# Performance work log

Measured on AMD Instinct MI355X. Metric: run time of the kernel, lower is better.

Reference implementation:

```python
import jax, jax.numpy as jnp
import numpy as np

DT = 1.0
BETA_E = float(np.exp(-DT / 20.0))
BETA_I = float(np.exp(-DT / 10.0))
ALPHA_E = float(np.exp(-DT / 5.0))
ALPHA_I = float(np.exp(-DT / 5.0))
R_E, R_I = 100.0, 100.0              # membrane resistance
U_REST_E, U_REST_I = -65.0, -65.0
THETA_E, THETA_I = -50.0, -50.0
U_RESET_E, U_RESET_I = -65.0, -65.0
E_WEIGHT, I_WEIGHT = 0.5, 2.0        # nn.Parameter scaling factors

B, T, N, N_IN = 8, 1000, 4096, 512


def setup_inputs() -> dict:
    key = jax.random.key(0)
    k1, k2, k3, k4 = jax.random.split(key, 4)
    neuron_types = jnp.where(jax.random.uniform(k1, (N,)) < 0.8, 1, -1).astype(jnp.int32)
    # non-negative connectome voxel counts, sparse-ish
    recurrent_weights = (jax.random.uniform(k2, (N, N)) * (jax.random.uniform(jax.random.fold_in(k2, 1), (N, N)) < 0.05)).astype(jnp.float32)
    feedforward_weights = jax.random.uniform(k3, (N_IN, N), dtype=jnp.float32)
    inputs = (jax.random.uniform(k4, (B, T, N_IN)) < 0.05).astype(jnp.float32)
    u_rest = jnp.where(neuron_types == 1, U_REST_E, U_REST_I).astype(jnp.float32)
    initial_v = jnp.broadcast_to(u_rest[None, :], (B, N)).astype(jnp.float32)
    initial_I = jnp.zeros((B, N), dtype=jnp.float32)
    return {
        "neuron_types": neuron_types,
        "recurrent_weights": recurrent_weights,
        "feedforward_weights": feedforward_weights,
        "inputs": inputs,
        "initial_v": initial_v,
        "initial_I": initial_I,
        "n_steps": T,
    }


def reference(neuron_types, recurrent_weights, feedforward_weights, inputs, initial_v, initial_I, n_steps):
    is_exc = (neuron_types == 1)
    f32 = jnp.float32
    beta = jnp.where(is_exc, BETA_E, BETA_I).astype(f32)      # (N,)
    alpha = jnp.where(is_exc, ALPHA_E, ALPHA_I).astype(f32)
    R = jnp.where(is_exc, R_E, R_I).astype(f32)
    u_rest = jnp.where(is_exc, U_REST_E, U_REST_I).astype(f32)
    theta = jnp.where(is_exc, THETA_E, THETA_I).astype(f32)
    u_reset = jnp.where(is_exc, U_RESET_E, U_RESET_I).astype(f32)
    # scaled_recurrent_weights: column j scaled by E_WEIGHT if post-column neuron j is exc
    scaling = jnp.where(is_exc, E_WEIGHT, I_WEIGHT).astype(f32)
    W = recurrent_weights * scaling[None, :]                   # (N, N)
    # precompute feedforward drive for all steps with one big GEMM: (B,T,Nin)@(Nin,N)
    drive = jnp.einsum('bti,in->btn', inputs, feedforward_weights)
    drive_t = jnp.transpose(drive, (1, 0, 2))                  # (T, B, N)

    def step(carry, drive_step):
        v, I = carry
        v = u_rest + (v - u_rest) * beta + I * (R * (1.0 - beta))
        s = (v >= theta).astype(f32)
        v = v * (1.0 - s) + u_reset * s
        I = I * alpha + s @ W + drive_step
        return (v, I), (s, v, I)

    _, (all_s, all_v, all_I) = jax.lax.scan(step, (initial_v, initial_I), drive_t, length=n_steps)
    # (T,B,N) -> (B,T,N)
    all_s = jnp.transpose(all_s, (1, 0, 2))
    all_v = jnp.transpose(all_v, (1, 0, 2))
    all_I = jnp.transpose(all_I, (1, 0, 2))
    return all_s, all_v, all_I
```

## Files before the change

kernel.cpp:

```cpp
#include <hip/hip_runtime.h>
#include <stdint.h>

#define N_NEUR 4096
#define N_IN   512
#define BATCH  8
#define TSTEPS 1000
#define KB_REC 128
#define KB_TOT 144
#define KB_PW  18
#define STRIDE_OUT (BATCH * TSTEPS * N_NEUR)

#define NCOPY   8
#define LSTRIDE 544

#define BETA_E_F 0.95122942450071400910f
#define BETA_I_F 0.90483741803595957316f
#define ALPHA_F  0.81873075307798185867f
#define RC_E_F   (100.0f * (1.0f - BETA_E_F))
#define RC_I_F   (100.0f * (1.0f - BETA_I_F))
#define U_REST_F  (-65.0f)
#define THETA_F   (-50.0f)
#define U_RESET_F (-65.0f)

typedef __attribute__((ext_vector_type(8))) short short8;
typedef __attribute__((ext_vector_type(4))) float f32x4;
typedef __attribute__((ext_vector_type(4))) int   i32x4;

__device__ __attribute__((aligned(16))) uint16_t g_B[256 * KB_TOT * 512];
__device__ __attribute__((aligned(4096))) unsigned long long g_spk[NCOPY][2][128 * LSTRIDE];
__device__ __attribute__((aligned(16))) uint8_t g_inb[TSTEPS * N_IN];
__device__ float g_I[BATCH * N_NEUR];
__device__ float g_vr[BATCH * N_NEUR];

__device__ __forceinline__ uint16_t f2bf(float v) {
    uint32_t x = __float_as_uint(v);
    uint32_t r = x + 0x7FFFu + ((x >> 16) & 1u);
    return (uint16_t)(r >> 16);
}
__device__ __forceinline__ uint32_t bswz(uint32_t x) {
    return (x & 0xFF0000FFu) | ((x & 0x0000FF00u) << 8) | ((x >> 8) & 0x0000FF00u);
}

__global__ void prep_w(const float* __restrict__ W, const int* __restrict__ types) {
    int o = blockIdx.x * 256 + threadIdx.x;
    int lane = o & 63, kb = (o >> 6) & 127, stripe = o >> 13;
    int col = (stripe << 4) + (lane & 15);
    float scale = (types[col] == 1) ? 0.5f : 2.0f;
    int kbase = kb * 32 + ((lane >> 4) & 3) * 8;
    uint32_t u[4];
#pragma unroll
    for (int p = 0; p < 4; ++p) {
        float v0 = W[(size_t)(kbase + 2 * p) * N_NEUR + col] * scale;
        float v1 = W[(size_t)(kbase + 2 * p + 1) * N_NEUR + col] * scale;
        u[p] = (uint32_t)f2bf(v0) | ((uint32_t)f2bf(v1) << 16);
    }
    i32x4 iv = { (int)u[0], (int)u[1], (int)u[2], (int)u[3] };
    ((short8*)g_B)[(stripe * KB_TOT + kb) * 64 + lane] = __builtin_bit_cast(short8, iv);
}

__global__ void prep_ff(const float* __restrict__ FF) {
    int o = blockIdx.x * 256 + threadIdx.x;
    int lane = o & 63, kbl = (o >> 6) & 15, stripe = o >> 10;
    int col = (stripe << 4) + (lane & 15);
    int kbase = kbl * 32 + ((lane >> 4) & 3) * 8;
    uint32_t u[4];
#pragma unroll
    for (int p = 0; p < 4; ++p) {
        float v0 = FF[(size_t)(kbase + 2 * p) * N_NEUR + col];
        float v1 = FF[(size_t)(kbase + 2 * p + 1) * N_NEUR + col];
        u[p] = (uint32_t)f2bf(v0) | ((uint32_t)f2bf(v1) << 16);
    }
    i32x4 iv = { (int)u[0], (int)u[1], (int)u[2], (int)u[3] };
    ((short8*)g_B)[(stripe * KB_TOT + 128 + kbl) * 64 + lane] = __builtin_bit_cast(short8, iv);
}

__global__ void prep_in(const float* __restrict__ inp) {
    const int total = TSTEPS * N_IN;
    for (int o = blockIdx.x * 256 + threadIdx.x; o < total; o += gridDim.x * 256) {
        int t = o >> 9, i = o & 511;
        uint32_t m = 0;
#pragma unroll
        for (int b = 0; b < 8; ++b) {
            float v = inp[(size_t)(b * TSTEPS + t) * N_IN + i];
            m |= (v != 0.0f ? 1u : 0u) << b;
        }
        g_inb[o] = (uint8_t)m;
    }
}

__global__ void k_zero() {
    int i = blockIdx.x * 256 + threadIdx.x;
    if (i < NCOPY * 2 * 1024) {
        int c = i >> 11;
        int p = (i >> 10) & 1;
        int wi = i & 1023;
        g_spk[c][p][(wi >> 3) * LSTRIDE + (wi & 7)] = 0ull;
    }
}

__global__ void k_init(const float* __restrict__ v0p, const float* __restrict__ I0p,
                       const int* __restrict__ types, float* __restrict__ out) {
    __shared__ uint8_t sb[256];
    int n = blockIdx.x * 256 + threadIdx.x;
    bool exc = (types[n] == 1);
    float beta = exc ? BETA_E_F : BETA_I_F;
    float rc   = exc ? RC_E_F   : RC_I_F;
    uint32_t bits = 0;
#pragma unroll
    for (int b = 0; b < 8; ++b) {
        int gi = b * N_NEUR + n;
        float v0 = v0p[gi], I0 = I0p[gi];
        float v = U_REST_F + (v0 - U_REST_F) * beta + I0 * rc;
        bool s = (v >= THETA_F);
        float vr = s ? U_RESET_F : v;
        out[(size_t)(b * TSTEPS + 0) * N_NEUR + n] = s ? 1.0f : 0.0f;
        out[STRIDE_OUT + (size_t)(b * TSTEPS + 0) * N_NEUR + n] = vr;
        g_vr[gi] = vr;
        g_I[gi]  = I0;
        bits |= (s ? 1u : 0u) << b;
    }
    sb[threadIdx.x] = (uint8_t)bits;
    __syncthreads();
    if (threadIdx.x < 64) {
        int l = threadIdx.x * 4;
        uint32_t w = (uint32_t)sb[l] | ((uint32_t)sb[l + 1] << 8)
                   | ((uint32_t)sb[l + 2] << 16) | ((uint32_t)sb[l + 3] << 24);
        int wi = blockIdx.x * 64 + threadIdx.x;
        int off = (wi >> 3) * LSTRIDE + (wi & 7);
        unsigned long long tg = (1ull << 32) | (unsigned long long)w;
#pragma unroll
        for (int c = 0; c < NCOPY; ++c) g_spk[c][1][off] = tg;
    }
}

__global__ void __launch_bounds__(512, 2)
k_persist(const int* __restrict__ types, float* __restrict__ out) {
    __shared__ __attribute__((aligned(16))) uint32_t swz[1152];
    __shared__ __attribute__((aligned(16))) float red[8][64][4];
    __shared__ unsigned long long wb[2];

    const int tid  = threadIdx.x;
    const int lane = tid & 63;
    const int w    = tid >> 6;
    const int blk  = blockIdx.x;
    const int stripe  = ((blk & 7) << 5) | (blk >> 3);
    const int colbase = stripe << 4;

    short8 Breg[KB_PW];
    {
        const short8* Bp = (const short8*)g_B + ((size_t)stripe * KB_TOT + w * KB_PW) * 64 + lane;
#pragma unroll
        for (int i = 0; i < KB_PW; ++i) Breg[i] = Bp[i * 64];
    }

    float Ireg = 0.f, vr = 0.f, beta = 0.f, rc = 0.f;
    int n = 0, b = 0;
    if (tid < 128) {
        b = tid >> 4;
        int nl = tid & 15;
        n = colbase + nl;
        int gi = b * N_NEUR + n;
        Ireg = g_I[gi];
        vr   = g_vr[gi];
        bool exc = (types[n] == 1);
        beta = exc ? BETA_E_F : BETA_I_F;
        rc   = exc ? RC_E_F   : RC_I_F;
    }

    const uint32_t msk = ((lane & 15) < 8) ? 0x00010001u : 0u;
    const int sA = lane & 7, sB = sA + 8;
    const int aoff = (lane >> 4) * 2;
    const int kb0 = w * KB_PW;

    const unsigned long long* const sp0 = g_spk[blk & 7][0];
    const unsigned long long* const sp1 = g_spk[blk & 7][1];
    const int a0 = ((tid >> 3) * LSTRIDE) | (tid & 7);
    const int a1 = (((tid + 512) >> 3) * LSTRIDE) | (tid & 7);

    for (int t = 1; t <= TSTEPS; ++t) {
        {
            const unsigned long long* sp = (t & 1) ? sp1 : sp0;
            unsigned long long v0 = 0, v1 = 0;
            bool d0 = false, d1 = false;
            while (true) {
                if (!d0) { v0 = __hip_atomic_load(&sp[a0], __ATOMIC_RELAXED, __HIP_MEMORY_SCOPE_AGENT);
                           d0 = ((uint32_t)(v0 >> 32) == (uint32_t)t); }
                if (!d1) { v1 = __hip_atomic_load(&sp[a1], __ATOMIC_RELAXED, __HIP_MEMORY_SCOPE_AGENT);
                           d1 = ((uint32_t)(v1 >> 32) == (uint32_t)t); }
                if (d0 && d1) break;
                __builtin_amdgcn_s_sleep(1);
            }
            swz[tid] = bswz((uint32_t)v0);
            swz[tid + 512] = bswz((uint32_t)v1);
            if (tid < 128) {
                uint32_t x = ((const uint32_t*)(g_inb + (size_t)(t - 1) * N_IN))[tid];
                swz[1024 + tid] = bswz(x);
            }
        }
        __syncthreads();

        f32x4 acc = {0.f, 0.f, 0.f, 0.f};
#pragma unroll
        for (int it = 0; it < KB_PW; ++it) {
            int kb = kb0 + it;
            uint32_t w0 = swz[kb * 8 + aoff];
            uint32_t w1 = swz[kb * 8 + aoff + 1];
            uint32_t a0v = ((w0 >> sA) & msk) * 0x3F80u;
            uint32_t a1v = ((w0 >> sB) & msk) * 0x3F80u;
            uint32_t a2v = ((w1 >> sA) & msk) * 0x3F80u;
            uint32_t a3v = ((w1 >> sB) & msk) * 0x3F80u;
            i32x4 ai = { (int)a0v, (int)a1v, (int)a2v, (int)a3v };
            short8 av = __builtin_bit_cast(short8, ai);
            acc = __builtin_amdgcn_mfma_f32_16x16x32_bf16(av, Breg[it], acc, 0, 0, 0);
        }
        *(f32x4*)&red[w][lane][0] = acc;
        __syncthreads();

        float Inew = 0.f, vn = 0.f;
        bool sbit = false;
        if (tid < 128) {
            int nl = tid & 15;
            int rl = (b >> 2) * 16 + nl, rr = b & 3;
            float S = 0.f;
#pragma unroll
            for (int q = 0; q < 8; ++q) S += red[q][rl][rr];
            Inew = Ireg * ALPHA_F + S;
            Ireg = Inew;
            if (t < TSTEPS) {
                float v = U_REST_F + (vr - U_REST_F) * beta + Inew * rc;
                sbit = (v >= THETA_F);
                vn = sbit ? U_RESET_F : v;
                vr = vn;
            }
            unsigned long long bal = __ballot(sbit);
            if ((tid & 63) == 0) wb[tid >> 6] = bal;
        }
        __syncthreads();

        if (t < TSTEPS && tid < 32) {
            unsigned long long b0 = wb[0], b1 = wb[1];
            const int j = tid & 3, c = tid >> 2;
            uint32_t word = 0;
#pragma unroll
            for (int u = 0; u < 4; ++u) {
                int nn = j * 4 + u;
                uint32_t byte = 0;
#pragma unroll
                for (int q = 0; q < 4; ++q) {
                    byte |= (uint32_t)((b0 >> (nn + 16 * q)) & 1ull) << q;
                    byte |= (uint32_t)((b1 >> (nn + 16 * q)) & 1ull) << (q + 4);
                }
                word |= byte << (8 * u);
            }
            unsigned long long tg = ((unsigned long long)(t + 1) << 32) | (unsigned long long)word;
            const int wi = stripe * 4 + j;
            __hip_atomic_store(&g_spk[c][(t + 1) & 1][(wi >> 3) * LSTRIDE + (wi & 7)], tg,
                               __ATOMIC_RELAXED, __HIP_MEMORY_SCOPE_AGENT);
        }
        if (tid < 128) {
            out[2 * STRIDE_OUT + (size_t)(b * TSTEPS + (t - 1)) * N_NEUR + n] = Inew;
            if (t < TSTEPS) {
                out[(size_t)(b * TSTEPS + t) * N_NEUR + n] = sbit ? 1.0f : 0.0f;
                out[STRIDE_OUT + (size_t)(b * TSTEPS + t) * N_NEUR + n] = vn;
            }
        }
    }
}

extern "C" void kernel_launch(void* const* d_in, const int* in_sizes, int n_in,
                              void* d_out, int out_size, void* d_ws, size_t ws_size,
                              hipStream_t stream) {
    const int*   types = (const int*)d_in[0];
    const float* Wrec  = (const float*)d_in[1];
    const float* FF    = (const float*)d_in[2];
    const float* inp   = (const float*)d_in[3];
    const float* v0    = (const float*)d_in[4];
    const float* I0    = (const float*)d_in[5];
    float* out = (float*)d_out;
    (void)in_sizes; (void)n_in; (void)out_size; (void)d_ws; (void)ws_size;

    hipLaunchKernelGGL(prep_w,  dim3(8192), dim3(256), 0, stream, Wrec, types);
    hipLaunchKernelGGL(prep_ff, dim3(1024), dim3(256), 0, stream, FF);
    hipLaunchKernelGGL(prep_in, dim3(512),  dim3(256), 0, stream, inp);
    hipLaunchKernelGGL(k_zero,  dim3(64),   dim3(256), 0, stream);
    hipLaunchKernelGGL(k_init,  dim3(16),   dim3(256), 0, stream, v0, I0, types, out);
    hipLaunchKernelGGL(k_persist, dim3(256), dim3(512), 0, stream, types, out);
}
```

Measured before the change: 3.850 ms.

## Per-wave spike polling without block barrier, more spike copies, split MFMA accumulators

Each wave now polls only the spike words its own K-slice needs and writes them to LDS itself. That replaces the block-wide __syncthreads before the MFMA loop with a wave-local LDS wait, and the sleep in the spin loop is removed. The number of replicated spike buffers rises from 8 to 16 to spread polling traffic across more copies, at the cost of more publisher stores per step. The MFMA chain is split across two accumulators to shorten the dependency chain, and the output stores become nontemporal to reduce cache pollution.

Result: slower. 4.122 ms (+7.1%).

```diff
diff --git a/kernel.cpp b/kernel.cpp
--- a/kernel.cpp
+++ b/kernel.cpp
@@ -10,7 +10,7 @@
 #define KB_PW  18
 #define STRIDE_OUT (BATCH * TSTEPS * N_NEUR)
 
-#define NCOPY   8
+#define NCOPY   16
 #define LSTRIDE 544
 
 #define BETA_E_F 0.95122942450071400910f
@@ -172,34 +172,53 @@
     const int aoff = (lane >> 4) * 2;
     const int kb0 = w * KB_PW;
 
-    const unsigned long long* const sp0 = g_spk[blk & 7][0];
-    const unsigned long long* const sp1 = g_spk[blk & 7][1];
-    const int a0 = ((tid >> 3) * LSTRIDE) | (tid & 7);
-    const int a1 = (((tid + 512) >> 3) * LSTRIDE) | (tid & 7);
+    const int base = w * KB_PW * 8;
+    const int idx0 = base + 2 * lane;
+    const int idx1 = idx0 + 1;
+    const bool has2 = (lane < 16);
+    const int idx2 = base + 128 + lane;
+    const bool tg0 = (idx0 < 1024);
+    const bool tg1 = (idx1 < 1024);
+    const bool tg2 = has2 && (idx2 < 1024);
+    const int po0 = (idx0 >> 3) * LSTRIDE + (idx0 & 7);
+    const int po1 = (idx1 >> 3) * LSTRIDE + (idx1 & 7);
+    const int po2 = (idx2 >> 3) * LSTRIDE + (idx2 & 7);
+
+    const unsigned long long* const sp0 = g_spk[blk & (NCOPY - 1)][0];
+    const unsigned long long* const sp1 = g_spk[blk & (NCOPY - 1)][1];
 
     for (int t = 1; t <= TSTEPS; ++t) {
+        const uint32_t* inw = (const uint32_t*)(g_inb + (size_t)(t - 1) * N_IN);
+        uint32_t x0 = 0, x1 = 0, x2 = 0;
+        if (!tg0) x0 = inw[idx0 - 1024];
+        if (!tg1) x1 = inw[idx1 - 1024];
+        if (has2 && !tg2) x2 = inw[idx2 - 1024];
+
         {
             const unsigned long long* sp = (t & 1) ? sp1 : sp0;
-            unsigned long long v0 = 0, v1 = 0;
-            bool d0 = false, d1 = false;
-            while (true) {
-                if (!d0) { v0 = __hip_atomic_load(&sp[a0], __ATOMIC_RELAXED, __HIP_MEMORY_SCOPE_AGENT);
+            unsigned long long v0 = 0, v1 = 0, v2 = 0;
+            bool d0 = !tg0, d1 = !tg1, d2 = !tg2;
+            while (!(d0 && d1 && d2)) {
+                if (!d0) { v0 = __hip_atomic_load(&sp[po0], __ATOMIC_RELAXED, __HIP_MEMORY_SCOPE_AGENT);
                            d0 = ((uint32_t)(v0 >> 32) == (uint32_t)t); }
-                if (!d1) { v1 = __hip_atomic_load(&sp[a1], __ATOMIC_RELAXED, __HIP_MEMORY_SCOPE_AGENT);
+                if (!d1) { v1 = __hip_atomic_load(&sp[po1], __ATOMIC_RELAXED, __HIP_MEMORY_SCOPE_AGENT);
                            d1 = ((uint32_t)(v1 >> 32) == (uint32_t)t); }
-                if (d0 && d1) break;
-                __builtin_amdgcn_s_sleep(1);
+                if (!d2) { v2 = __hip_atomic_load(&sp[po2], __ATOMIC_RELAXED, __HIP_MEMORY_SCOPE_AGENT);
+                           d2 = ((uint32_t)(v2 >> 32) == (uint32_t)t); }
             }
-            swz[tid] = bswz((uint32_t)v0);
-            swz[tid + 512] = bswz((uint32_t)v1);
-            if (tid < 128) {
-                uint32_t x = ((const uint32_t*)(g_inb + (size_t)(t - 1) * N_IN))[tid];
-                swz[1024 + tid] = bswz(x);
-            }
-        }
-        __syncthreads();
-
-        f32x4 acc = {0.f, 0.f, 0.f, 0.f};
+            if (tg0) x0 = (uint32_t)v0;
+            if (tg1) x1 = (uint32_t)v1;
+            if (tg2) x2 = (uint32_t)v2;
+        }
+
+        swz[idx0] = bswz(x0);
+        swz[idx1] = bswz(x1);
+        if (has2) swz[idx2] = bswz(x2);
+        asm volatile("s_waitcnt lgkmcnt(0)" ::: "memory");
+        __builtin_amdgcn_sched_barrier(0);
+
+        f32x4 acc0 = {0.f, 0.f, 0.f, 0.f};
+        f32x4 acc1 = {0.f, 0.f, 0.f, 0.f};
 #pragma unroll
         for (int it = 0; it < KB_PW; ++it) {
             int kb = kb0 + it;
@@ -211,8 +230,10 @@
             uint32_t a3v = ((w1 >> sB) & msk) * 0x3F80u;
             i32x4 ai = { (int)a0v, (int)a1v, (int)a2v, (int)a3v };
             short8 av = __builtin_bit_cast(short8, ai);
-            acc = __builtin_amdgcn_mfma_f32_16x16x32_bf16(av, Breg[it], acc, 0, 0, 0);
-        }
+            if (it & 1) acc1 = __builtin_amdgcn_mfma_f32_16x16x32_bf16(av, Breg[it], acc1, 0, 0, 0);
+            else        acc0 = __builtin_amdgcn_mfma_f32_16x16x32_bf16(av, Breg[it], acc0, 0, 0, 0);
+        }
+        f32x4 acc = acc0 + acc1;
         *(f32x4*)&red[w][lane][0] = acc;
         __syncthreads();
 
@@ -237,7 +258,7 @@
         }
         __syncthreads();
 
-        if (t < TSTEPS && tid < 32) {
+        if (t < TSTEPS && tid < 4 * NCOPY) {
             unsigned long long b0 = wb[0], b1 = wb[1];
             const int j = tid & 3, c = tid >> 2;
             uint32_t word = 0;
@@ -258,10 +279,10 @@
                                __ATOMIC_RELAXED, __HIP_MEMORY_SCOPE_AGENT);
         }
         if (tid < 128) {
-            out[2 * STRIDE_OUT + (size_t)(b * TSTEPS + (t - 1)) * N_NEUR + n] = Inew;
+            __builtin_nontemporal_store(Inew, &out[2 * STRIDE_OUT + (size_t)(b * TSTEPS + (t - 1)) * N_NEUR + n]);
             if (t < TSTEPS) {
-                out[(size_t)(b * TSTEPS + t) * N_NEUR + n] = sbit ? 1.0f : 0.0f;
-                out[STRIDE_OUT + (size_t)(b * TSTEPS + t) * N_NEUR + n] = vn;
+                __builtin_nontemporal_store(sbit ? 1.0f : 0.0f, &out[(size_t)(b * TSTEPS + t) * N_NEUR + n]);
+                __builtin_nontemporal_store(vn, &out[STRIDE_OUT + (size_t)(b * TSTEPS + t) * N_NEUR + n]);
             }
         }
     }
@@ -282,7 +303,7 @@
     hipLaunchKernelGGL(prep_w,  dim3(8192), dim3(256), 0, stream, Wrec, types);
     hipLaunchKernelGGL(prep_ff, dim3(1024), dim3(256), 0, stream, FF);
     hipLaunchKernelGGL(prep_in, dim3(512),  dim3(256), 0, stream, inp);
-    hipLaunchKernelGGL(k_zero,  dim3(64),   dim3(256), 0, stream);
+    hipLaunchKernelGGL(k_zero,  dim3(128),  dim3(256), 0, stream);
     hipLaunchKernelGGL(k_init,  dim3(16),   dim3(256), 0, stream, v0, I0, types, out);
     hipLaunchKernelGGL(k_persist, dim3(256), dim3(512), 0, stream, types, out);
 }
```

## Remap neuron-thread layout to pack spikes per wave, dropping a barrier and splitting MFMA accumulators

Applied to the files above, without the earlier changes.

Threads are remapped so each wave holds 8 neurons across all 8 batches. Each wave can then pack its own ballot into spike words with a multiply bit-gather and publish them directly. This removes the shared-memory ballot buffer and one __syncthreads per timestep on the serial critical path. The MFMA chain is also split into three independent accumulators to shorten the dependency latency. In exchange, the output stores become less coalesced, since consecutive lanes now stride across batch rows.

Result: slower. 4.221 ms (+9.7%).

```diff
diff --git a/kernel.cpp b/kernel.cpp
--- a/kernel.cpp
+++ b/kernel.cpp
@@ -137,7 +137,6 @@
 k_persist(const int* __restrict__ types, float* __restrict__ out) {
     __shared__ __attribute__((aligned(16))) uint32_t swz[1152];
     __shared__ __attribute__((aligned(16))) float red[8][64][4];
-    __shared__ unsigned long long wb[2];
 
     const int tid  = threadIdx.x;
     const int lane = tid & 63;
@@ -154,11 +153,11 @@
     }
 
     float Ireg = 0.f, vr = 0.f, beta = 0.f, rc = 0.f;
-    int n = 0, b = 0;
+    int n = 0, b = 0, c16 = 0;
     if (tid < 128) {
-        b = tid >> 4;
-        int nl = tid & 15;
-        n = colbase + nl;
+        b   = lane >> 3;
+        c16 = (tid >> 6) * 8 + (lane & 7);
+        n   = colbase + c16;
         int gi = b * N_NEUR + n;
         Ireg = g_I[gi];
         vr   = g_vr[gi];
@@ -172,8 +171,8 @@
     const int aoff = (lane >> 4) * 2;
     const int kb0 = w * KB_PW;
 
-    const unsigned long long* const sp0 = g_spk[blk & 7][0];
-    const unsigned long long* const sp1 = g_spk[blk & 7][1];
+    const unsigned long long* const sp0 = g_spk[blk & (NCOPY - 1)][0];
+    const unsigned long long* const sp1 = g_spk[blk & (NCOPY - 1)][1];
     const int a0 = ((tid >> 3) * LSTRIDE) | (tid & 7);
     const int a1 = (((tid + 512) >> 3) * LSTRIDE) | (tid & 7);
 
@@ -199,7 +198,9 @@
         }
         __syncthreads();
 
-        f32x4 acc = {0.f, 0.f, 0.f, 0.f};
+        f32x4 acc0 = {0.f, 0.f, 0.f, 0.f};
+        f32x4 acc1 = {0.f, 0.f, 0.f, 0.f};
+        f32x4 acc2 = {0.f, 0.f, 0.f, 0.f};
 #pragma unroll
         for (int it = 0; it < KB_PW; ++it) {
             int kb = kb0 + it;
@@ -211,16 +212,19 @@
             uint32_t a3v = ((w1 >> sB) & msk) * 0x3F80u;
             i32x4 ai = { (int)a0v, (int)a1v, (int)a2v, (int)a3v };
             short8 av = __builtin_bit_cast(short8, ai);
-            acc = __builtin_amdgcn_mfma_f32_16x16x32_bf16(av, Breg[it], acc, 0, 0, 0);
-        }
+            int ch = it - (it / 3) * 3;
+            if (ch == 0)      acc0 = __builtin_amdgcn_mfma_f32_16x16x32_bf16(av, Breg[it], acc0, 0, 0, 0);
+            else if (ch == 1) acc1 = __builtin_amdgcn_mfma_f32_16x16x32_bf16(av, Breg[it], acc1, 0, 0, 0);
+            else              acc2 = __builtin_amdgcn_mfma_f32_16x16x32_bf16(av, Breg[it], acc2, 0, 0, 0);
+        }
+        f32x4 acc = (acc0 + acc1) + acc2;
         *(f32x4*)&red[w][lane][0] = acc;
         __syncthreads();
 
-        float Inew = 0.f, vn = 0.f;
-        bool sbit = false;
         if (tid < 128) {
-            int nl = tid & 15;
-            int rl = (b >> 2) * 16 + nl, rr = b & 3;
+            float Inew, vn = 0.f;
+            bool sbit = false;
+            const int rl = ((b >> 2) << 4) + c16, rr = b & 3;
             float S = 0.f;
 #pragma unroll
             for (int q = 0; q < 8; ++q) S += red[q][rl][rr];
@@ -233,31 +237,20 @@
                 vr = vn;
             }
             unsigned long long bal = __ballot(sbit);
-            if ((tid & 63) == 0) wb[tid >> 6] = bal;
-        }
-        __syncthreads();
-
-        if (t < TSTEPS && tid < 32) {
-            unsigned long long b0 = wb[0], b1 = wb[1];
-            const int j = tid & 3, c = tid >> 2;
-            uint32_t word = 0;
-#pragma unroll
-            for (int u = 0; u < 4; ++u) {
-                int nn = j * 4 + u;
-                uint32_t byte = 0;
-#pragma unroll
-                for (int q = 0; q < 4; ++q) {
-                    byte |= (uint32_t)((b0 >> (nn + 16 * q)) & 1ull) << q;
-                    byte |= (uint32_t)((b1 >> (nn + 16 * q)) & 1ull) << (q + 4);
+            if (t < TSTEPS && lane < 16) {
+                const int j2 = lane & 1, c = lane >> 1;
+                uint32_t word = 0;
+#pragma unroll
+                for (int m = 0; m < 4; ++m) {
+                    unsigned long long tt = (bal >> (4 * j2 + m)) & 0x0101010101010101ull;
+                    uint32_t byte = (uint32_t)((tt * 0x0102040810204080ull) >> 56);
+                    word |= byte << (8 * m);
                 }
-                word |= byte << (8 * u);
-            }
-            unsigned long long tg = ((unsigned long long)(t + 1) << 32) | (unsigned long long)word;
-            const int wi = stripe * 4 + j;
-            __hip_atomic_store(&g_spk[c][(t + 1) & 1][(wi >> 3) * LSTRIDE + (wi & 7)], tg,
-                               __ATOMIC_RELAXED, __HIP_MEMORY_SCOPE_AGENT);
-        }
-        if (tid < 128) {
+                unsigned long long tg = ((unsigned long long)(t + 1) << 32) | (unsigned long long)word;
+                const int wi = stripe * 4 + (tid >> 6) * 2 + j2;
+                __hip_atomic_store(&g_spk[c][(t + 1) & 1][(wi >> 3) * LSTRIDE + (wi & 7)], tg,
+                                   __ATOMIC_RELAXED, __HIP_MEMORY_SCOPE_AGENT);
+            }
             out[2 * STRIDE_OUT + (size_t)(b * TSTEPS + (t - 1)) * N_NEUR + n] = Inew;
             if (t < TSTEPS) {
                 out[(size_t)(b * TSTEPS + t) * N_NEUR + n] = sbit ? 1.0f : 0.0f;
```
